# Optimization experiments

Hardware: AMD Instinct MI355X
Metric: run time of the kernel (lower is better)

## Reference

```python
import jax, jax.numpy as jnp
import numpy as np

VOC_SIZE = 1_000_000
EMBED_DIM = 64
N_UPD = 262_144
B, L = 4096, 200


def setup_inputs() -> dict:
    key = jax.random.key(0)
    k1, k2, k3, k4 = jax.random.split(key, 4)
    kernel = jax.random.normal(k1, (VOC_SIZE, EMBED_DIM), dtype=jnp.float32)
    indices = jax.random.randint(k2, (N_UPD,), 0, VOC_SIZE, dtype=jnp.int64)
    emb_update = jax.random.normal(k3, (N_UPD, EMBED_DIM), dtype=jnp.float32)
    qs = jax.random.randint(k4, (B, L), 0, VOC_SIZE, dtype=jnp.int64)
    return {"kernel": kernel, "indices": indices, "emb_update": emb_update, "qs": qs}


def reference(kernel, indices, emb_update, qs):
    # tf.scatter_add: kernel[indices[i]] += emb_update[i] (duplicate indices accumulate)
    updated = kernel.at[indices].add(emb_update)
    # K.gather: rows of the updated table at qs -> shape qs.shape + (embed_dim,)
    return updated[qs]
```

## Files before the change

kernel.cpp:

```cpp
#include <hip/hip_runtime.h>


#define EMBED_DIM 64

__global__ void scatter_add_kernel(float* __restrict__ table,
                                   const int* __restrict__ indices,
                                   const float* __restrict__ upd,
                                   int total ) {
    int tid = blockIdx.x * blockDim.x + threadIdx.x;
    if (tid >= total) return;
    int i = tid >> 6;
    int d = tid & 63;
    int row = indices[i];
    atomicAdd(&table[(size_t)row * EMBED_DIM + d], upd[tid]);
}

__global__ void gather_kernel(const float4* __restrict__ table,
                              const int* __restrict__ qs,
                              float4* __restrict__ out,
                              int total ) {
    int tid = blockIdx.x * blockDim.x + threadIdx.x;
    if (tid >= total) return;
    int r = tid >> 4;
    int c = tid & 15;
    int q = qs[r];
    out[tid] = table[q * 16 + c];
}

extern "C" void kernel_launch(void* const* d_in, const int* in_sizes, int n_in,
                              void* d_out, int out_size, void* d_ws, size_t ws_size,
                              hipStream_t stream) {
    float* table = (float*)d_in[0];
    const int* indices = (const int*)d_in[1];
    const float* upd = (const float*)d_in[2];
    const int* qs = (const int*)d_in[3];
    float* out = (float*)d_out;

    const int n_upd = in_sizes[1];
    const int n_q = in_sizes[3];

    const int scatter_total = n_upd * EMBED_DIM;
    const int gather_total = n_q * (EMBED_DIM / 4);

    const int block = 256;
    scatter_add_kernel<<<(scatter_total + block - 1) / block, block, 0, stream>>>(
        table, indices, upd, scatter_total);
    gather_kernel<<<(gather_total + block - 1) / block, block, 0, stream>>>(
        (const float4*)table, qs, (float4*)out, gather_total);
}
```

Measured before the change: 472.8 us.

## Accumulate scatter updates in a workspace hash table and fuse them into the gather

Instead of atomically adding updates into the embedding table in place, the launch builds an open-addressing hash table of the updated rows in the workspace, accumulates the updates into a compact delta buffer, and has the gather probe the hash and add the delta. The input table is no longer mutated, and the scatter atomics land in a smaller contiguous buffer. In exchange it adds extra kernel launches, zeroing of keys and delta rows, and a hash probe plus a conditional delta read on every gathered row. The path runs only if the workspace holds roughly 264 MB; otherwise the old two-kernel path is used.

```diff
diff --git a/kernel.cpp b/kernel.cpp
--- a/kernel.cpp
+++ b/kernel.cpp
@@ -1,12 +1,87 @@
 #include <hip/hip_runtime.h>
+#include <stdint.h>
 
 
 #define EMBED_DIM 64
+#define NSLOT_LOG 20
+#define NSLOT (1u << NSLOT_LOG)
+#define HMASK (NSLOT - 1u)
+
+__device__ __forceinline__ unsigned hash_row(unsigned row) {
+    return (row * 2654435761u) >> (32 - NSLOT_LOG);
+}
+
+__global__ void zero_keys_kernel(uint4* __restrict__ keys4, int n4) {
+    int t = blockIdx.x * blockDim.x + threadIdx.x;
+    if (t < n4) keys4[t] = make_uint4(0u, 0u, 0u, 0u);
+}
+
+__global__ void build_hash_kernel(const int* __restrict__ indices,
+                                  unsigned* __restrict__ keys,
+                                  int* __restrict__ slot_of,
+                                  float4* __restrict__ delta,
+                                  int n_upd) {
+    int i = blockIdx.x * blockDim.x + threadIdx.x;
+    if (i >= n_upd) return;
+    unsigned row = (unsigned)indices[i];
+    unsigned key = row + 1u;
+    unsigned p = hash_row(row);
+    for (;;) {
+        unsigned old = atomicCAS(&keys[p], 0u, key);
+        if (old == 0u || old == key) break;
+        p = (p + 1u) & HMASK;
+    }
+    slot_of[i] = (int)p;
+    float4 z = make_float4(0.f, 0.f, 0.f, 0.f);
+    float4* drow = delta + ((size_t)p << 4);
+#pragma unroll
+    for (int c = 0; c < 16; ++c) drow[c] = z;
+}
+
+__global__ void accumulate_kernel(const float* __restrict__ upd,
+                                  const int* __restrict__ slot_of,
+                                  float* __restrict__ delta,
+                                  int total ) {
+    int tid = blockIdx.x * blockDim.x + threadIdx.x;
+    if (tid >= total) return;
+    int i = tid >> 6;
+    int d = tid & 63;
+    int slot = slot_of[i];
+    atomicAdd(&delta[((size_t)slot << 6) + d], upd[tid]);
+}
+
+__global__ void gather_fused_kernel(const float4* __restrict__ table,
+                                    const int* __restrict__ qs,
+                                    const unsigned* __restrict__ keys,
+                                    const float4* __restrict__ delta,
+                                    float4* __restrict__ out,
+                                    int total ) {
+    int tid = blockIdx.x * blockDim.x + threadIdx.x;
+    if (tid >= total) return;
+    int r = tid >> 4;
+    int c = tid & 15;
+    unsigned row = (unsigned)qs[r];
+    unsigned key = row + 1u;
+    unsigned p = hash_row(row);
+    int slot = -1;
+    for (;;) {
+        unsigned k = keys[p];
+        if (k == key) { slot = (int)p; break; }
+        if (k == 0u) break;
+        p = (p + 1u) & HMASK;
+    }
+    float4 v = table[((size_t)row << 4) + c];
+    if (slot >= 0) {
+        float4 dv = delta[((size_t)slot << 4) + c];
+        v.x += dv.x; v.y += dv.y; v.z += dv.z; v.w += dv.w;
+    }
+    out[tid] = v;
+}
 
 __global__ void scatter_add_kernel(float* __restrict__ table,
                                    const int* __restrict__ indices,
                                    const float* __restrict__ upd,
-                                   int total ) {
+                                   int total) {
     int tid = blockIdx.x * blockDim.x + threadIdx.x;
     if (tid >= total) return;
     int i = tid >> 6;
@@ -18,7 +93,7 @@
 __global__ void gather_kernel(const float4* __restrict__ table,
                               const int* __restrict__ qs,
                               float4* __restrict__ out,
-                              int total ) {
+                              int total) {
     int tid = blockIdx.x * blockDim.x + threadIdx.x;
     if (tid >= total) return;
     int r = tid >> 4;
@@ -30,7 +105,7 @@
 extern "C" void kernel_launch(void* const* d_in, const int* in_sizes, int n_in,
                               void* d_out, int out_size, void* d_ws, size_t ws_size,
                               hipStream_t stream) {
-    float* table = (float*)d_in[0];
+    const float* table = (const float*)d_in[0];
     const int* indices = (const int*)d_in[1];
     const float* upd = (const float*)d_in[2];
     const int* qs = (const int*)d_in[3];
@@ -38,13 +113,39 @@
 
     const int n_upd = in_sizes[1];
     const int n_q = in_sizes[3];
+    const int block = 256;
 
-    const int scatter_total = n_upd * EMBED_DIM;
-    const int gather_total = n_q * (EMBED_DIM / 4);
+    const size_t keys_bytes  = (size_t)NSLOT * 4;
+    const size_t delta_off   = 8u * 1024u * 1024u;
+    const size_t need = delta_off + (size_t)NSLOT * EMBED_DIM * 4;
 
-    const int block = 256;
-    scatter_add_kernel<<<(scatter_total + block - 1) / block, block, 0, stream>>>(
-        table, indices, upd, scatter_total);
-    gather_kernel<<<(gather_total + block - 1) / block, block, 0, stream>>>(
-        (const float4*)table, qs, (float4*)out, gather_total);
+    if (ws_size >= need) {
+        unsigned* keys = (unsigned*)d_ws;
+        int* slot_of   = (int*)((char*)d_ws + keys_bytes);
+        float* delta   = (float*)((char*)d_ws + delta_off);
+
+        const int nkeys4 = (int)(NSLOT / 4);
+        zero_keys_kernel<<<(nkeys4 + block - 1) / block, block, 0, stream>>>(
+            (uint4*)keys, nkeys4);
+
+        build_hash_kernel<<<(n_upd + block - 1) / block, block, 0, stream>>>(
+            indices, keys, slot_of, (float4*)delta, n_upd);
+
+        const int acc_total = n_upd * EMBED_DIM;
+        accumulate_kernel<<<(acc_total + block - 1) / block, block, 0, stream>>>(
+            upd, slot_of, delta, acc_total);
+
+        const int gat_total = n_q * (EMBED_DIM / 4);
+        gather_fused_kernel<<<(gat_total + block - 1) / block, block, 0, stream>>>(
+            (const float4*)table, qs, keys, (const float4*)delta,
+            (float4*)out, gat_total);
+    } else {
+        float* mtable = (float*)d_in[0];
+        const int scatter_total = n_upd * EMBED_DIM;
+        const int gather_total = n_q * (EMBED_DIM / 4);
+        scatter_add_kernel<<<(scatter_total + block - 1) / block, block, 0, stream>>>(
+            mtable, indices, upd, scatter_total);
+        gather_kernel<<<(gather_total + block - 1) / block, block, 0, stream>>>(
+            (const float4*)mtable, qs, (float4*)out, gather_total);
+    }
 }
```

Measured after the change: 524.4 us. 10.9% more time.
